# Kernel optimization log

Measured on AMD Instinct MI355X. Metric: run time of the kernel, lower is better.

The kernel has to match this reference:

```python
import jax, jax.numpy as jnp
import numpy as np

N = 50000   # nodes
E = 600000  # edges (avg degree 12)
D = 128     # node feature dim (input == hidden so residual applies)
R = 7       # num_relation
G = 32      # num graphs in the batch
L = 3       # layers
W_SCALE = 0.02


def setup_inputs() -> dict:
    key = jax.random.key(0)
    ks = jax.random.split(key, 5 + 2 * L)
    inp = {
        "x": jax.random.normal(ks[0], (N, D), jnp.float32),
        "node_in": jax.random.randint(ks[1], (E,), 0, N),
        "node_out": jax.random.randint(ks[2], (E,), 0, N),
        "relation": jax.random.randint(ks[3], (E,), 0, R),
        "edge_weight": jnp.ones((E,), jnp.float32),
        "node2graph": jnp.sort(jax.random.randint(ks[4], (N,), 0, G)),
        "num_node": N,
        "num_graphs": G,
    }
    for i in range(L):
        inp[f"sl_w{i}"] = jax.random.normal(ks[5 + 2 * i], (D, D), jnp.float32) * W_SCALE
        inp[f"sl_b{i}"] = jnp.zeros((D,), jnp.float32)
        inp[f"lin_w{i}"] = jax.random.normal(ks[6 + 2 * i], (R * D, D), jnp.float32) * W_SCALE
        inp[f"lin_b{i}"] = jnp.zeros((D,), jnp.float32)
    return inp


def _gearnet(x, edge_weight, params, node_in, node_out, relation, node2graph,
             num_node, num_graphs):
    # relation-keyed scatter index: node_out * R + relation
    idx = node_out * R + relation  # [E]
    h = x
    for (sl_w, sl_b, lin_w, lin_b) in params:
        din = h.shape[1]
        msg = h[node_in] * edge_weight[:, None]                           # [E, din] gather
        agg = jax.ops.segment_sum(msg, idx, num_segments=num_node * R)    # [N*R, din] scatter_add
        upd = agg.reshape(num_node, R * din)                              # [N, R*din]
        out = jax.nn.relu(upd @ lin_w + lin_b + h @ sl_w + sl_b)          # combine: linear + self_loop, relu
        h = out + h                                                        # short_cut residual (shapes match)
    node_feature = h
    graph_feature = jax.ops.segment_sum(node_feature, node2graph, num_segments=num_graphs)  # SumReadout
    return graph_feature, node_feature


def reference(x, node_in, node_out, relation, edge_weight, node2graph,
              sl_w0, sl_b0, lin_w0, lin_b0,
              sl_w1, sl_b1, lin_w1, lin_b1,
              sl_w2, sl_b2, lin_w2, lin_b2,
              num_node, num_graphs):
    params = [(sl_w0, sl_b0, lin_w0, lin_b0),
              (sl_w1, sl_b1, lin_w1, lin_b1),
              (sl_w2, sl_b2, lin_w2, lin_b2)]
    return _gearnet(x, edge_weight, params, node_in, node_out, relation,
                    node2graph, num_node, num_graphs)
```

## Files before the change

kernel.cpp:

```cpp
#include <hip/hip_runtime.h>
#include <hip/hip_bf16.h>

#define NN 50000
#define EE 600000
#define DD 128
#define RR 7
#define GG 32
#define NB1 ((NN + 1023) / 1024)

typedef float f32x4 __attribute__((ext_vector_type(4)));
typedef float f32x2 __attribute__((ext_vector_type(2)));
typedef short short8 __attribute__((ext_vector_type(8)));

static __device__ __forceinline__ unsigned short f2bf(float f) {
    union { float f; unsigned u; } v; v.f = f;
    unsigned r = v.u + 0x7fff + ((v.u >> 16) & 1);
    return (unsigned short)(r >> 16);
}
static __device__ __forceinline__ float bf2f(unsigned short u) {
    union { unsigned u; float f; } v; v.u = ((unsigned)u) << 16;
    return v.f;
}

__global__ void prep_w2(const float* lw0, const float* lw1, const float* lw2,
                        const float* sw0, const float* sw1, const float* sw2,
                        const float* lb0, const float* lb1, const float* lb2,
                        const float* sb0, const float* sb1, const float* sb2,
                        unsigned short* __restrict__ Wt2, float* __restrict__ bias) {
    int l = blockIdx.x >> 9;
    int idx = (blockIdx.x & 511) * 256 + threadIdx.x;
    const float* lin_w = l == 0 ? lw0 : (l == 1 ? lw1 : lw2);
    const float* sl_w  = l == 0 ? sw0 : (l == 1 ? sw1 : sw2);
    if (idx < DD) {
        const float* lin_b = l == 0 ? lb0 : (l == 1 ? lb1 : lb2);
        const float* sl_b  = l == 0 ? sb0 : (l == 1 ? sb1 : sb2);
        bias[l * DD + idx] = lin_b[idx] + sl_b[idx];
    }
    if (idx >= 1024 * DD) return;
    int j = idx >> 7;
    int k = idx & 127;
    int slot = j >> 7, dout = j & 127;
    float w = (slot < 7) ? lin_w[(slot * DD + k) * DD + dout] : sl_w[k * DD + dout];
    Wt2[(size_t)l * 1024 * DD + (size_t)j * DD + k] = f2bf(w);
}

__global__ void zero_misc(int* __restrict__ cc, int* __restrict__ slop, float* __restrict__ gf) {
    int i = blockIdx.x * 256 + threadIdx.x;
    if (i < 2 * NN) cc[i] = 0;
    if (i < 16) slop[i] = 0;
    if (i < GG * DD) gf[i] = 0.f;
}

__global__ void hist(const int* __restrict__ node_out, int* __restrict__ counts) {
    int e = blockIdx.x * 256 + threadIdx.x;
    if (e >= EE) return;
    atomicAdd(&counts[node_out[e]], 1);
}

__global__ __launch_bounds__(256) void scan1(const int* __restrict__ counts,
                                             int* __restrict__ start, int* __restrict__ bsum) {
    __shared__ int s[256];
    int tid = threadIdx.x;
    int base = blockIdx.x * 1024 + tid * 4;
    int v[4], sum = 0;
    #pragma unroll
    for (int j = 0; j < 4; ++j) {
        v[j] = (base + j < NN) ? counts[base + j] : 0;
        sum += v[j];
    }
    s[tid] = sum; __syncthreads();
    for (int off = 1; off < 256; off <<= 1) {
        int t = (tid >= off) ? s[tid - off] : 0;
        __syncthreads();
        s[tid] += t;
        __syncthreads();
    }
    int run = s[tid] - sum;
    if (tid == 255) bsum[blockIdx.x] = s[255];
    #pragma unroll
    for (int j = 0; j < 4; ++j) {
        if (base + j < NN) { start[base + j] = run; run += v[j]; }
    }
}

__global__ __launch_bounds__(64) void scan2(int* __restrict__ bsum) {
    __shared__ int s[64];
    int tid = threadIdx.x;
    int v = (tid < NB1) ? bsum[tid] : 0;
    s[tid] = v; __syncthreads();
    for (int off = 1; off < 64; off <<= 1) {
        int t = (tid >= off) ? s[tid - off] : 0;
        __syncthreads();
        s[tid] += t;
        __syncthreads();
    }
    if (tid < NB1) bsum[tid] = s[tid] - v;
}

__global__ void scan3(const int* __restrict__ start, const int* __restrict__ bsum,
                      const int* __restrict__ counts, int2* __restrict__ segd) {
    int i = blockIdx.x * 256 + threadIdx.x;
    if (i < NN) segd[i] = make_int2(start[i] + bsum[i >> 10], counts[i]);
}

__global__ void fill(const int* __restrict__ node_in, const int* __restrict__ node_out,
                     const int* __restrict__ rel, const float* __restrict__ ew,
                     const int2* __restrict__ segd, int* __restrict__ cursor,
                     int2* __restrict__ edges) {
    int e = blockIdx.x * 256 + threadIdx.x;
    if (e >= EE) return;
    int seg = node_out[e];
    int pos = segd[seg].x + atomicAdd(&cursor[seg], 1);
    edges[pos] = make_int2((rel[e] << 16) | node_in[e], __float_as_int(ew[e]));
}

__global__ void init_hb(const float* __restrict__ x, unsigned short* __restrict__ hb) {
    int t = blockIdx.x * 256 + threadIdx.x;
    if (t >= NN * 32) return;
    f32x4 v = ((const f32x4*)x)[t];
    unsigned long long pack = (unsigned long long)f2bf(v.x)
                            | ((unsigned long long)f2bf(v.y) << 16)
                            | ((unsigned long long)f2bf(v.z) << 32)
                            | ((unsigned long long)f2bf(v.w) << 48);
    ((unsigned long long*)hb)[t] = pack;
}

__global__ __launch_bounds__(256) void gemm_p(
        const unsigned short* __restrict__ hb,
        const unsigned short* __restrict__ Wt2,
        unsigned short* __restrict__ P) {
    int tid = threadIdx.x;
    int wid = tid >> 6, lane = tid & 63;
    int wr = wid >> 1, wc = wid & 1;
    int lm = lane & 15, lg = lane >> 4;
    int bm0 = blockIdx.x * 128;

    short8 af[4][4];
    #pragma unroll
    for (int mi = 0; mi < 4; ++mi) {
        int gr = bm0 + wr * 64 + mi * 16 + lm;
        #pragma unroll
        for (int ks = 0; ks < 4; ++ks) {
            short8 t = {};
            if (gr < NN) t = *(const short8*)(hb + (size_t)gr * DD + ks * 32 + lg * 8);
            af[mi][ks] = t;
        }
    }
    for (int cb = 0; cb < 8; ++cb) {
        f32x4 acc[4][4] = {};
        #pragma unroll
        for (int ks = 0; ks < 4; ++ks) {
            short8 bfr[4];
            #pragma unroll
            for (int ni = 0; ni < 4; ++ni)
                bfr[ni] = *(const short8*)(Wt2 + (size_t)(cb * 128 + wc * 64 + ni * 16 + lm) * DD
                                           + ks * 32 + lg * 8);
            #pragma unroll
            for (int mi = 0; mi < 4; ++mi)
                #pragma unroll
                for (int ni = 0; ni < 4; ++ni)
                    acc[mi][ni] = __builtin_amdgcn_mfma_f32_16x16x32_bf16(af[mi][ks], bfr[ni], acc[mi][ni], 0, 0, 0);
        }
        #pragma unroll
        for (int mi = 0; mi < 4; ++mi) {
            #pragma unroll
            for (int v = 0; v < 4; ++v) {
                int gm = bm0 + wr * 64 + mi * 16 + lg * 4 + v;
                if (gm >= NN) continue;
                #pragma unroll
                for (int ni = 0; ni < 4; ++ni) {
                    int j = cb * 128 + wc * 64 + ni * 16 + lm;
                    P[(size_t)gm * 1024 + j] = f2bf(acc[mi][ni][v]);
                }
            }
        }
    }
}

#define PR(r) ((const uint2*)(P + (size_t)(((((r).x & 0xFFFF) << 3) | ((r).x >> 16))) * DD) + l5)
__global__ __launch_bounds__(256) void gather_p(
        const unsigned short* __restrict__ P,
        const int2* __restrict__ segd,
        const int2* __restrict__ edges,
        const float* __restrict__ bias,
        const unsigned short* __restrict__ hb_in,
        unsigned short* __restrict__ hb_out,
        float* __restrict__ nf,
        int last) {
    int tid = threadIdx.x;
    int wv = tid >> 6, lane = tid & 63;
    int h = lane >> 5, l5 = lane & 31;
    int node = blockIdx.x * 4 + wv;
    int2 sd = segd[node];
    int st = sd.x, cnt = sd.y;
    int base = st + h;
    int mmax = (cnt + 1) >> 1;

    f32x4 ac = {0.f, 0.f, 0.f, 0.f};
    int2 r0 = edges[base];
    int2 r1 = edges[base + 2];
    int2 r2 = edges[base + 4];
    uint2 hv0 = *PR(r0);
    uint2 hv1 = *PR(r1);
    for (int i = 0; i < mmax; ++i) {
        int2 r3 = edges[base + 2 * i + 6];
        uint2 hv2 = *PR(r2);
        if (h + 2 * i < cnt) {
            float w = __int_as_float(r0.y);
            ac.x += bf2f((unsigned short)(hv0.x & 0xFFFF)) * w;
            ac.y += bf2f((unsigned short)(hv0.x >> 16)) * w;
            ac.z += bf2f((unsigned short)(hv0.y & 0xFFFF)) * w;
            ac.w += bf2f((unsigned short)(hv0.y >> 16)) * w;
        }
        r0 = r1; r1 = r2; r2 = r3;
        hv0 = hv1; hv1 = hv2;
    }
    ac.x += __shfl_xor(ac.x, 32);
    ac.y += __shfl_xor(ac.y, 32);
    ac.z += __shfl_xor(ac.z, 32);
    ac.w += __shfl_xor(ac.w, 32);

    if (h == 0) {
        uint2 hs = *((const uint2*)(P + ((size_t)node * 8 + 7) * DD) + l5);
        f32x4 b4 = ((const f32x4*)bias)[l5];
        uint2 hp = ((const uint2*)hb_in)[(size_t)node * 32 + l5];
        float o0 = fmaxf(ac.x + bf2f((unsigned short)(hs.x & 0xFFFF)) + b4.x, 0.f) + bf2f((unsigned short)(hp.x & 0xFFFF));
        float o1 = fmaxf(ac.y + bf2f((unsigned short)(hs.x >> 16))   + b4.y, 0.f) + bf2f((unsigned short)(hp.x >> 16));
        float o2 = fmaxf(ac.z + bf2f((unsigned short)(hs.y & 0xFFFF)) + b4.z, 0.f) + bf2f((unsigned short)(hp.y & 0xFFFF));
        float o3 = fmaxf(ac.w + bf2f((unsigned short)(hs.y >> 16))   + b4.w, 0.f) + bf2f((unsigned short)(hp.y >> 16));
        if (last) {
            ((f32x4*)nf)[(size_t)node * 32 + l5] = (f32x4){o0, o1, o2, o3};
        } else {
            uint2 pk;
            pk.x = (unsigned)f2bf(o0) | ((unsigned)f2bf(o1) << 16);
            pk.y = (unsigned)f2bf(o2) | ((unsigned)f2bf(o3) << 16);
            ((uint2*)hb_out)[(size_t)node * 32 + l5] = pk;
        }
    }
}

__global__ __launch_bounds__(256) void readout(const float* __restrict__ h,
                                               const int* __restrict__ n2g,
                                               float* __restrict__ gf) {
    int c0 = blockIdx.x * 128;
    int rg = threadIdx.x >> 5, d4 = threadIdx.x & 31;
    f32x4 acc = {0.f, 0.f, 0.f, 0.f};
    int cur = -1;
    #pragma unroll 4
    for (int it = 0; it < 16; ++it) {
        int row = c0 + it * 8 + rg;
        if (row >= NN) break;
        int g = n2g[row];
        if (g != cur) {
            if (cur >= 0) {
                atomicAdd(&gf[cur * DD + d4 * 4 + 0], acc.x);
                atomicAdd(&gf[cur * DD + d4 * 4 + 1], acc.y);
                atomicAdd(&gf[cur * DD + d4 * 4 + 2], acc.z);
                atomicAdd(&gf[cur * DD + d4 * 4 + 3], acc.w);
            }
            cur = g;
            acc = (f32x4){0.f, 0.f, 0.f, 0.f};
        }
        acc += ((const f32x4*)h)[(size_t)row * 32 + d4];
    }
    if (cur >= 0) {
        atomicAdd(&gf[cur * DD + d4 * 4 + 0], acc.x);
        atomicAdd(&gf[cur * DD + d4 * 4 + 1], acc.y);
        atomicAdd(&gf[cur * DD + d4 * 4 + 2], acc.z);
        atomicAdd(&gf[cur * DD + d4 * 4 + 3], acc.w);
    }
}

extern "C" void kernel_launch(void* const* d_in, const int* in_sizes, int n_in,
                              void* d_out, int out_size, void* d_ws, size_t ws_size,
                              hipStream_t stream) {
    const float* x      = (const float*)d_in[0];
    const int* node_in  = (const int*)d_in[1];
    const int* node_out = (const int*)d_in[2];
    const int* relation = (const int*)d_in[3];
    const float* ew     = (const float*)d_in[4];
    const int* n2g      = (const int*)d_in[5];

    float* out = (float*)d_out;
    float* gf = out;
    float* nf = out + GG * DD;

    char* ws = (char*)d_ws;
    size_t off = 0;
    unsigned short* P  = (unsigned short*)(ws + off); off += (size_t)NN * 1024 * 2;
    unsigned short* hb0 = (unsigned short*)(ws + off); off += (size_t)NN * DD * 2;
    unsigned short* hb1 = (unsigned short*)(ws + off); off += (size_t)NN * DD * 2;
    unsigned short* Wt2 = (unsigned short*)(ws + off); off += (size_t)3 * 1024 * DD * 2;
    float* bias = (float*)(ws + off);            off += 3 * DD * 4;
    int* counts = (int*)(ws + off);              off += (size_t)NN * 4;
    int* cursor = (int*)(ws + off);              off += (size_t)NN * 4;
    int* start  = (int*)(ws + off);              off += (size_t)NN * 4;
    int2* segd  = (int2*)(ws + off);             off += (size_t)NN * 8;
    int* bsum   = (int*)(ws + off);              off += 64 * 4;
    int2* edges = (int2*)(ws + off);             off += (size_t)(EE + 8) * 8;

    prep_w2<<<3 * 512, 256, 0, stream>>>(
        (const float*)d_in[10], (const float*)d_in[14], (const float*)d_in[18],
        (const float*)d_in[8],  (const float*)d_in[12], (const float*)d_in[16],
        (const float*)d_in[11], (const float*)d_in[15], (const float*)d_in[19],
        (const float*)d_in[9],  (const float*)d_in[13], (const float*)d_in[17],
        Wt2, bias);

    zero_misc<<<(2 * NN + 255) / 256, 256, 0, stream>>>(counts, (int*)(edges + EE), gf);
    hist<<<(EE + 255) / 256, 256, 0, stream>>>(node_out, counts);
    scan1<<<NB1, 256, 0, stream>>>(counts, start, bsum);
    scan2<<<1, 64, 0, stream>>>(bsum);
    scan3<<<(NN + 255) / 256, 256, 0, stream>>>(start, bsum, counts, segd);
    fill<<<(EE + 255) / 256, 256, 0, stream>>>(node_in, node_out, relation, ew,
                                               segd, cursor, edges);
    init_hb<<<(NN * 32) / 256, 256, 0, stream>>>(x, hb0);

    unsigned short* hbs[2] = { hb0, hb1 };
    for (int l = 0; l < 3; ++l) {
        gemm_p<<<(NN + 127) / 128, 256, 0, stream>>>(
            hbs[l & 1], Wt2 + (size_t)l * 1024 * DD, P);
        gather_p<<<NN / 4, 256, 0, stream>>>(
            P, segd, edges, bias + l * DD, hbs[l & 1], hbs[(l + 1) & 1],
            nf, l == 2 ? 1 : 0);
    }
    readout<<<(NN + 127) / 128, 256, 0, stream>>>(nf, n2g, gf);
}
```

Baseline: 364.3 us.

## Widen gather to 16-byte loads with four edge lanes; fuse x conversion

The gather kernel now splits each wave into four groups of 16 lanes. Each lane loads 8 bf16 values (16 bytes) per edge, so four edges are processed in parallel with a cross-lane reduction over both halves. The separate init_hb conversion kernel is removed: the first GEMM converts fp32 x to bf16 on the fly, and the first gather reads the fp32 x residual directly. This cuts one launch and one pass over x and gives wider memory transactions, at the cost of extra shuffles and more padding in the edge list.

```diff
diff --git a/kernel.cpp b/kernel.cpp
--- a/kernel.cpp
+++ b/kernel.cpp
@@ -9,8 +9,8 @@
 #define NB1 ((NN + 1023) / 1024)
 
 typedef float f32x4 __attribute__((ext_vector_type(4)));
-typedef float f32x2 __attribute__((ext_vector_type(2)));
 typedef short short8 __attribute__((ext_vector_type(8)));
+typedef unsigned u32x4 __attribute__((ext_vector_type(4)));
 
 static __device__ __forceinline__ unsigned short f2bf(float f) {
     union { float f; unsigned u; } v; v.f = f;
@@ -47,7 +47,7 @@
 __global__ void zero_misc(int* __restrict__ cc, int* __restrict__ slop, float* __restrict__ gf) {
     int i = blockIdx.x * 256 + threadIdx.x;
     if (i < 2 * NN) cc[i] = 0;
-    if (i < 16) slop[i] = 0;
+    if (i < 32) slop[i] = 0;
     if (i < GG * DD) gf[i] = 0.f;
 }
 
@@ -114,19 +114,9 @@
     edges[pos] = make_int2((rel[e] << 16) | node_in[e], __float_as_int(ew[e]));
 }
 
-__global__ void init_hb(const float* __restrict__ x, unsigned short* __restrict__ hb) {
-    int t = blockIdx.x * 256 + threadIdx.x;
-    if (t >= NN * 32) return;
-    f32x4 v = ((const f32x4*)x)[t];
-    unsigned long long pack = (unsigned long long)f2bf(v.x)
-                            | ((unsigned long long)f2bf(v.y) << 16)
-                            | ((unsigned long long)f2bf(v.z) << 32)
-                            | ((unsigned long long)f2bf(v.w) << 48);
-    ((unsigned long long*)hb)[t] = pack;
-}
-
 __global__ __launch_bounds__(256) void gemm_p(
         const unsigned short* __restrict__ hb,
+        const float* __restrict__ xf,
         const unsigned short* __restrict__ Wt2,
         unsigned short* __restrict__ P) {
     int tid = threadIdx.x;
@@ -136,14 +126,34 @@
     int bm0 = blockIdx.x * 128;
 
     short8 af[4][4];
-    #pragma unroll
-    for (int mi = 0; mi < 4; ++mi) {
-        int gr = bm0 + wr * 64 + mi * 16 + lm;
-        #pragma unroll
-        for (int ks = 0; ks < 4; ++ks) {
-            short8 t = {};
-            if (gr < NN) t = *(const short8*)(hb + (size_t)gr * DD + ks * 32 + lg * 8);
-            af[mi][ks] = t;
+    if (xf) {
+        #pragma unroll
+        for (int mi = 0; mi < 4; ++mi) {
+            int gr = bm0 + wr * 64 + mi * 16 + lm;
+            #pragma unroll
+            for (int ks = 0; ks < 4; ++ks) {
+                short8 t = {};
+                if (gr < NN) {
+                    f32x4 a0 = *(const f32x4*)(xf + (size_t)gr * DD + ks * 32 + lg * 8);
+                    f32x4 a1 = *(const f32x4*)(xf + (size_t)gr * DD + ks * 32 + lg * 8 + 4);
+                    t[0] = (short)f2bf(a0.x); t[1] = (short)f2bf(a0.y);
+                    t[2] = (short)f2bf(a0.z); t[3] = (short)f2bf(a0.w);
+                    t[4] = (short)f2bf(a1.x); t[5] = (short)f2bf(a1.y);
+                    t[6] = (short)f2bf(a1.z); t[7] = (short)f2bf(a1.w);
+                }
+                af[mi][ks] = t;
+            }
+        }
+    } else {
+        #pragma unroll
+        for (int mi = 0; mi < 4; ++mi) {
+            int gr = bm0 + wr * 64 + mi * 16 + lm;
+            #pragma unroll
+            for (int ks = 0; ks < 4; ++ks) {
+                short8 t = {};
+                if (gr < NN) t = *(const short8*)(hb + (size_t)gr * DD + ks * 32 + lg * 8);
+                af[mi][ks] = t;
+            }
         }
     }
     for (int cb = 0; cb < 8; ++cb) {
@@ -177,64 +187,85 @@
     }
 }
 
-#define PR(r) ((const uint2*)(P + (size_t)(((((r).x & 0xFFFF) << 3) | ((r).x >> 16))) * DD) + l5)
+#define PR4(r) (((const u32x4*)(P + (size_t)(((((r).x & 0xFFFF) << 3) | ((r).x >> 16))) * DD)) + l4)
 __global__ __launch_bounds__(256) void gather_p(
         const unsigned short* __restrict__ P,
         const int2* __restrict__ segd,
         const int2* __restrict__ edges,
         const float* __restrict__ bias,
         const unsigned short* __restrict__ hb_in,
+        const float* __restrict__ xf,
         unsigned short* __restrict__ hb_out,
         float* __restrict__ nf,
         int last) {
     int tid = threadIdx.x;
     int wv = tid >> 6, lane = tid & 63;
-    int h = lane >> 5, l5 = lane & 31;
+    int q = lane >> 4, l4 = lane & 15;
     int node = blockIdx.x * 4 + wv;
     int2 sd = segd[node];
     int st = sd.x, cnt = sd.y;
-    int base = st + h;
-    int mmax = (cnt + 1) >> 1;
-
-    f32x4 ac = {0.f, 0.f, 0.f, 0.f};
+    int base = st + q;
+    int mmax = (cnt + 3) >> 2;
+
+    float ac[8] = {};
     int2 r0 = edges[base];
-    int2 r1 = edges[base + 2];
-    int2 r2 = edges[base + 4];
-    uint2 hv0 = *PR(r0);
-    uint2 hv1 = *PR(r1);
+    int2 r1 = edges[base + 4];
+    int2 r2 = edges[base + 8];
+    u32x4 hv0 = *PR4(r0);
+    u32x4 hv1 = *PR4(r1);
     for (int i = 0; i < mmax; ++i) {
-        int2 r3 = edges[base + 2 * i + 6];
-        uint2 hv2 = *PR(r2);
-        if (h + 2 * i < cnt) {
+        int2 r3 = edges[base + 4 * i + 12];
+        u32x4 hv2 = *PR4(r2);
+        if (q + 4 * i < cnt) {
             float w = __int_as_float(r0.y);
-            ac.x += bf2f((unsigned short)(hv0.x & 0xFFFF)) * w;
-            ac.y += bf2f((unsigned short)(hv0.x >> 16)) * w;
-            ac.z += bf2f((unsigned short)(hv0.y & 0xFFFF)) * w;
-            ac.w += bf2f((unsigned short)(hv0.y >> 16)) * w;
+            #pragma unroll
+            for (int j = 0; j < 4; ++j) {
+                ac[2 * j]     += bf2f((unsigned short)(hv0[j] & 0xFFFF)) * w;
+                ac[2 * j + 1] += bf2f((unsigned short)(hv0[j] >> 16)) * w;
+            }
         }
         r0 = r1; r1 = r2; r2 = r3;
         hv0 = hv1; hv1 = hv2;
     }
-    ac.x += __shfl_xor(ac.x, 32);
-    ac.y += __shfl_xor(ac.y, 32);
-    ac.z += __shfl_xor(ac.z, 32);
-    ac.w += __shfl_xor(ac.w, 32);
-
-    if (h == 0) {
-        uint2 hs = *((const uint2*)(P + ((size_t)node * 8 + 7) * DD) + l5);
-        f32x4 b4 = ((const f32x4*)bias)[l5];
-        uint2 hp = ((const uint2*)hb_in)[(size_t)node * 32 + l5];
-        float o0 = fmaxf(ac.x + bf2f((unsigned short)(hs.x & 0xFFFF)) + b4.x, 0.f) + bf2f((unsigned short)(hp.x & 0xFFFF));
-        float o1 = fmaxf(ac.y + bf2f((unsigned short)(hs.x >> 16))   + b4.y, 0.f) + bf2f((unsigned short)(hp.x >> 16));
-        float o2 = fmaxf(ac.z + bf2f((unsigned short)(hs.y & 0xFFFF)) + b4.z, 0.f) + bf2f((unsigned short)(hp.y & 0xFFFF));
-        float o3 = fmaxf(ac.w + bf2f((unsigned short)(hs.y >> 16))   + b4.w, 0.f) + bf2f((unsigned short)(hp.y >> 16));
+    #pragma unroll
+    for (int j = 0; j < 8; ++j) {
+        ac[j] += __shfl_xor(ac[j], 16);
+        ac[j] += __shfl_xor(ac[j], 32);
+    }
+    if (q == 0) {
+        u32x4 hs = ((const u32x4*)(P + ((size_t)node * 8 + 7) * DD))[l4];
+        f32x4 b0 = ((const f32x4*)bias)[l4 * 2];
+        f32x4 b1 = ((const f32x4*)bias)[l4 * 2 + 1];
+        float hp[8];
+        if (xf) {
+            f32x4 h0 = ((const f32x4*)xf)[(size_t)node * 32 + l4 * 2];
+            f32x4 h1 = ((const f32x4*)xf)[(size_t)node * 32 + l4 * 2 + 1];
+            hp[0] = h0.x; hp[1] = h0.y; hp[2] = h0.z; hp[3] = h0.w;
+            hp[4] = h1.x; hp[5] = h1.y; hp[6] = h1.z; hp[7] = h1.w;
+        } else {
+            u32x4 hpv = ((const u32x4*)hb_in)[(size_t)node * 16 + l4];
+            #pragma unroll
+            for (int j = 0; j < 4; ++j) {
+                hp[2 * j]     = bf2f((unsigned short)(hpv[j] & 0xFFFF));
+                hp[2 * j + 1] = bf2f((unsigned short)(hpv[j] >> 16));
+            }
+        }
+        float bb[8] = { b0.x, b0.y, b0.z, b0.w, b1.x, b1.y, b1.z, b1.w };
+        float o[8];
+        #pragma unroll
+        for (int j = 0; j < 4; ++j) {
+            o[2 * j]     = fmaxf(ac[2 * j]     + bf2f((unsigned short)(hs[j] & 0xFFFF)) + bb[2 * j],     0.f) + hp[2 * j];
+            o[2 * j + 1] = fmaxf(ac[2 * j + 1] + bf2f((unsigned short)(hs[j] >> 16))    + bb[2 * j + 1], 0.f) + hp[2 * j + 1];
+        }
         if (last) {
-            ((f32x4*)nf)[(size_t)node * 32 + l5] = (f32x4){o0, o1, o2, o3};
+            ((f32x4*)nf)[(size_t)node * 32 + l4 * 2]     = (f32x4){o[0], o[1], o[2], o[3]};
+            ((f32x4*)nf)[(size_t)node * 32 + l4 * 2 + 1] = (f32x4){o[4], o[5], o[6], o[7]};
         } else {
-            uint2 pk;
-            pk.x = (unsigned)f2bf(o0) | ((unsigned)f2bf(o1) << 16);
-            pk.y = (unsigned)f2bf(o2) | ((unsigned)f2bf(o3) << 16);
-            ((uint2*)hb_out)[(size_t)node * 32 + l5] = pk;
+            u32x4 pk;
+            #pragma unroll
+            for (int j = 0; j < 4; ++j)
+                pk[j] = (unsigned)f2bf(o[2 * j]) | ((unsigned)f2bf(o[2 * j + 1]) << 16);
+            ((u32x4*)hb_out)[(size_t)node * 16 + l4] = pk;
         }
     }
 }
@@ -297,7 +328,7 @@
     int* start  = (int*)(ws + off);              off += (size_t)NN * 4;
     int2* segd  = (int2*)(ws + off);             off += (size_t)NN * 8;
     int* bsum   = (int*)(ws + off);              off += 64 * 4;
-    int2* edges = (int2*)(ws + off);             off += (size_t)(EE + 8) * 8;
+    int2* edges = (int2*)(ws + off);             off += (size_t)(EE + 16) * 8;
 
     prep_w2<<<3 * 512, 256, 0, stream>>>(
         (const float*)d_in[10], (const float*)d_in[14], (const float*)d_in[18],
@@ -313,15 +344,16 @@
     scan3<<<(NN + 255) / 256, 256, 0, stream>>>(start, bsum, counts, segd);
     fill<<<(EE + 255) / 256, 256, 0, stream>>>(node_in, node_out, relation, ew,
                                                segd, cursor, edges);
-    init_hb<<<(NN * 32) / 256, 256, 0, stream>>>(x, hb0);
-
-    unsigned short* hbs[2] = { hb0, hb1 };
-    for (int l = 0; l < 3; ++l) {
-        gemm_p<<<(NN + 127) / 128, 256, 0, stream>>>(
-            hbs[l & 1], Wt2 + (size_t)l * 1024 * DD, P);
-        gather_p<<<NN / 4, 256, 0, stream>>>(
-            P, segd, edges, bias + l * DD, hbs[l & 1], hbs[(l + 1) & 1],
-            nf, l == 2 ? 1 : 0);
-    }
+
+    gemm_p<<<(NN + 127) / 128, 256, 0, stream>>>(nullptr, x, Wt2, P);
+    gather_p<<<NN / 4, 256, 0, stream>>>(P, segd, edges, bias, nullptr, x,
+                                         hb1, nf, 0);
+    gemm_p<<<(NN + 127) / 128, 256, 0, stream>>>(hb1, nullptr, Wt2 + (size_t)1024 * DD, P);
+    gather_p<<<NN / 4, 256, 0, stream>>>(P, segd, edges, bias + DD, hb1, nullptr,
+                                         hb0, nf, 0);
+    gemm_p<<<(NN + 127) / 128, 256, 0, stream>>>(hb0, nullptr, Wt2 + (size_t)2048 * DD, P);
+    gather_p<<<NN / 4, 256, 0, stream>>>(P, segd, edges, bias + 2 * DD, hb0, nullptr,
+                                         nullptr, nf, 1);
+
     readout<<<(NN + 127) / 128, 256, 0, stream>>>(nf, n2g, gf);
 }
```

Result: no change. 358.9 us (median of 2 runs) (-1.5%).
